# Kernel optimization log

Hardware: AMD Instinct MI355X
Metric: run time of the kernel (lower is better)

## Reference

```python
import jax, jax.numpy as jnp
import numpy as np

S, B, C, H = 1024, 4, 1024, 16
CC = C // H


def setup_inputs() -> dict:
    key = jax.random.key(0)
    k0, k1, k2, k3, k4, k5 = jax.random.split(key, 6)
    x = jax.random.normal(k0, (S, B, C), jnp.float32)
    pe = jax.random.normal(k1, (S, B, C), jnp.float32)
    # causal content mask: True = masked (query i cannot attend key j > i)
    causal = np.triu(np.ones((S, S), dtype=bool), 1)
    content_mask = jnp.asarray(np.broadcast_to(causal[:, :, None], (S, S, B)))
    # per-batch tail padding; every sequence has >= 512 valid tokens
    lengths = np.array([S, S - 128, S - 256, S - 512])
    padding_mask = jnp.asarray(np.arange(S)[:, None] >= lengths[None, :])  # [s, b]
    sc = 1.0 / np.sqrt(C).astype(np.float32)
    Wqkv = jax.random.normal(k2, (3 * C, C), jnp.float32) * sc
    bqkv = jax.random.normal(k3, (3 * C,), jnp.float32) * 0.01
    Wo = jax.random.normal(k4, (C, C), jnp.float32) * sc
    bo = jax.random.normal(k5, (C,), jnp.float32) * 0.01
    return {"x": x, "pe": pe, "content_mask": content_mask,
            "padding_mask": padding_mask, "Wqkv": Wqkv, "bqkv": bqkv,
            "Wo": Wo, "bo": bo}


def reference(x, pe, content_mask, padding_mask, Wqkv, bqkv, Wo, bo):
    s, b, c = x.shape
    qkv = (x + pe) @ Wqkv.T + bqkv                       # [s, b, 3c]
    q, k, v = jnp.split(qkv, 3, axis=-1)
    q = q.reshape(s, b, H, CC)
    k = k.reshape(s, b, H, CC)
    v = v.reshape(s, b, H, CC)
    temperature = 1.0 / np.sqrt(CC).astype(np.float32)
    qk = jnp.einsum('sbhc,tbhc->stbh', q, k) * temperature  # [s, t, b, h]
    mask = content_mask[:, :, :, None] | padding_mask[None, :, :, None]
    a = jnp.where(mask, -jnp.inf, qk)
    p = jax.nn.softmax(a, axis=1)                        # softmax over key dim t
    out = jnp.einsum('stbh,tbhc->sbhc', p, v).reshape(s, b, c)
    return out @ Wo.T + bo
```

## Files before the change

kernel.cpp:

```cpp
#include <hip/hip_runtime.h>
#include <hip/hip_bf16.h>

#define S_  1024
#define B_  4
#define C_  1024
#define H_  16
#define CC_ 64
#define M_  (S_ * B_)
#define N_QKV (3 * C_)

typedef __bf16 bf16x8 __attribute__((ext_vector_type(8)));
typedef __bf16 bf16x4 __attribute__((ext_vector_type(4)));
typedef float  f32x4  __attribute__((ext_vector_type(4)));

__device__ __forceinline__ void gload16(const void* g, void* l) {
    __builtin_amdgcn_global_load_lds(
        (const __attribute__((address_space(1))) void*)g,
        (__attribute__((address_space(3))) void*)l, 16, 0, 0);
}

__global__ void prep_kernel(const float* __restrict__ x, const float* __restrict__ pe,
                            const float* __restrict__ Wqkv, const float* __restrict__ Wo,
                            __bf16* __restrict__ xpe, __bf16* __restrict__ wq,
                            __bf16* __restrict__ wo) {
    int bid = blockIdx.x;
    int t = threadIdx.x;
    if (bid < 4096) {
        int i = bid * 256 + t;
        float4 a = ((const float4*)x)[i];
        float4 p = ((const float4*)pe)[i];
        bf16x4 r;
        r[0] = (__bf16)(a.x + p.x); r[1] = (__bf16)(a.y + p.y);
        r[2] = (__bf16)(a.z + p.z); r[3] = (__bf16)(a.w + p.w);
        ((bf16x4*)xpe)[i] = r;
    } else if (bid < 7168) {
        int i = (bid - 4096) * 256 + t;
        float4 a = ((const float4*)Wqkv)[i];
        bf16x4 r;
        r[0] = (__bf16)a.x; r[1] = (__bf16)a.y; r[2] = (__bf16)a.z; r[3] = (__bf16)a.w;
        ((bf16x4*)wq)[i] = r;
    } else {
        int i = (bid - 7168) * 256 + t;
        float4 a = ((const float4*)Wo)[i];
        bf16x4 r;
        r[0] = (__bf16)a.x; r[1] = (__bf16)a.y; r[2] = (__bf16)a.z; r[3] = (__bf16)a.w;
        ((bf16x4*)wo)[i] = r;
    }
}

template<int EPI, int BN>
__global__ __launch_bounds__(256, 2)
void gemm_bt_kernel(const __bf16* __restrict__ A, const __bf16* __restrict__ B,
                    const float* __restrict__ bias, int M, int N, int K,
                    float* __restrict__ Cf, __bf16* __restrict__ Cq,
                    __bf16* __restrict__ Vt) {
    constexpr int NB = BN / 32;
    __shared__ __bf16 Als[128 * 32];
    __shared__ __bf16 Bls[BN * 32];

    const int tid  = threadIdx.x;
    const int lane = tid & 63;
    const int wid  = tid >> 6;
    const int quad = lane >> 4;
    const int l15  = lane & 15;
    const int wm   = wid >> 1;
    const int wn   = wid & 1;
    const int m0   = blockIdx.y * 128;
    const int n0   = blockIdx.x * BN;

    const int u0 = tid, u1 = 256 + tid;
    const int row0 = u0 >> 2, ch0 = (u0 & 3) * 8;
    const int row1 = u1 >> 2, ch1 = (u1 & 3) * 8;
    char* lA0 = (char*)Als + (size_t)(wid * 64) * 16;
    char* lA1 = (char*)Als + (size_t)(256 + wid * 64) * 16;
    char* lB0 = (char*)Bls + (size_t)(wid * 64) * 16;
    char* lB1 = (char*)Bls + (size_t)(256 + wid * 64) * 16;

    f32x4 acc[4][NB];
#pragma unroll
    for (int i = 0; i < 4; i++)
#pragma unroll
        for (int j = 0; j < NB; j++) acc[i][j] = f32x4{0.f, 0.f, 0.f, 0.f};

    for (int k0 = 0; k0 < K; k0 += 32) {
        __syncthreads();
        gload16(&A[(size_t)(m0 + row0) * K + k0 + ch0], lA0);
        gload16(&A[(size_t)(m0 + row1) * K + k0 + ch1], lA1);
        gload16(&B[(size_t)(n0 + row0) * K + k0 + ch0], lB0);
        if (BN == 128)
            gload16(&B[(size_t)(n0 + row1) * K + k0 + ch1], lB1);
        __syncthreads();

        bf16x8 af[4], bfr[NB];
#pragma unroll
        for (int mb = 0; mb < 4; mb++)
            af[mb] = *(const bf16x8*)&Als[(wm * 64 + mb * 16 + l15) * 32 + quad * 8];
#pragma unroll
        for (int nb = 0; nb < NB; nb++)
            bfr[nb] = *(const bf16x8*)&Bls[(wn * (BN / 2) + nb * 16 + l15) * 32 + quad * 8];

#pragma unroll
        for (int mb = 0; mb < 4; mb++)
#pragma unroll
            for (int nb = 0; nb < NB; nb++)
                acc[mb][nb] = __builtin_amdgcn_mfma_f32_16x16x32_bf16(
                    af[mb], bfr[nb], acc[mb][nb], 0, 0, 0);
    }

#pragma unroll
    for (int mb = 0; mb < 4; mb++) {
#pragma unroll
        for (int nb = 0; nb < NB; nb++) {
#pragma unroll
            for (int r = 0; r < 4; r++) {
                int m = m0 + wm * 64 + mb * 16 + quad * 4 + r;
                int n = n0 + wn * (BN / 2) + nb * 16 + l15;
                float v = acc[mb][nb][r] + bias[n];
                if (EPI == 0) {
                    Cf[(size_t)m * N + n] = v;
                } else {
                    int sec = n >> 10;
                    int c   = n & 1023;
                    int h   = c >> 6;
                    int cc  = c & 63;
                    int s   = m >> 2;
                    int b   = m & 3;
                    if (sec == 2) {
                        size_t off = ((size_t)(b * H_ + h) * CC_ + cc) * S_ + s;
                        Vt[off] = (__bf16)v;
                    } else {
                        size_t off = ((((size_t)(sec * B_ + b) * H_ + h) * S_ + s) << 6) + cc;
                        Cq[off] = (__bf16)v;
                    }
                }
            }
        }
    }
}

__global__ __launch_bounds__(256, 4)
void attn_kernel(const __bf16* __restrict__ qkv, const __bf16* __restrict__ vt,
                 __bf16* __restrict__ att) {
    const int qt  = 15 - blockIdx.x;
    const int bh  = blockIdx.y;
    const int b   = bh >> 4;
    const int h   = bh & 15;
    const int len = 1024 - ((b == 1) ? 128 : (b == 2) ? 256 : (b == 3) ? 512 : 0);

    const int tid  = threadIdx.x;
    const int w    = tid >> 6;
    const int lane = tid & 63;
    const int quad = lane >> 4;
    const int l15  = lane & 15;
    const int qbase = qt * 64;

    const size_t head  = ((size_t)(b * H_ + h)) * S_ * CC_;
    const size_t plane = (size_t)B_ * H_ * S_ * CC_;
    const __bf16* qg  = qkv + head;
    const __bf16* kg  = qkv + plane + head;
    const __bf16* vtg = vt + (size_t)bh * CC_ * S_;

    const int qw = qbase + w * 16;
    const int q  = qw + l15;
    bf16x8 qf0 = *(const bf16x8*)&qg[(size_t)q * 64 + quad * 8];
    bf16x8 qf1 = *(const bf16x8*)&qg[(size_t)q * 64 + 32 + quad * 8];

    __shared__ __bf16 Kls[64 * 72];
    __shared__ __bf16 Vtls[64 * 72];
    __shared__ __bf16 Pls[4 * 16 * 72];
    __bf16* pw = &Pls[w * 16 * 72];

    f32x4 oacc[4];
#pragma unroll
    for (int cb = 0; cb < 4; cb++) oacc[cb] = f32x4{0.f, 0.f, 0.f, 0.f};
    float m_i = -1e30f, l_i = 0.f;

    const int kend_blk = min(qbase + 64, len);
    const int kend_w   = min(qw + 16, len);
    const float temp = 0.125f;

    const int r0 = tid >> 3,          c0 = (tid & 7) * 8;
    const int r1 = (256 + tid) >> 3,  c1 = (tid & 7) * 8;

    for (int t0 = 0; t0 < kend_blk; t0 += 64) {
        __syncthreads();
        *(bf16x8*)&Kls[r0 * 72 + c0]  = *(const bf16x8*)&kg[(size_t)(t0 + r0) * 64 + c0];
        *(bf16x8*)&Kls[r1 * 72 + c1]  = *(const bf16x8*)&kg[(size_t)(t0 + r1) * 64 + c1];
        *(bf16x8*)&Vtls[r0 * 72 + c0] = *(const bf16x8*)&vtg[(size_t)r0 * S_ + t0 + c0];
        *(bf16x8*)&Vtls[r1 * 72 + c1] = *(const bf16x8*)&vtg[(size_t)r1 * S_ + t0 + c1];
        __syncthreads();
        if (t0 >= kend_w) continue;

        f32x4 sc[4];
#pragma unroll
        for (int nb = 0; nb < 4; nb++) {
            bf16x8 kf0 = *(const bf16x8*)&Kls[(nb * 16 + l15) * 72 + quad * 8];
            bf16x8 kf1 = *(const bf16x8*)&Kls[(nb * 16 + l15) * 72 + 32 + quad * 8];
            f32x4 s = f32x4{0.f, 0.f, 0.f, 0.f};
            s = __builtin_amdgcn_mfma_f32_16x16x32_bf16(kf0, qf0, s, 0, 0, 0);
            s = __builtin_amdgcn_mfma_f32_16x16x32_bf16(kf1, qf1, s, 0, 0, 0);
            sc[nb] = s;
        }
        if (t0 + 64 <= qw) {
#pragma unroll
            for (int nb = 0; nb < 4; nb++)
#pragma unroll
                for (int r = 0; r < 4; r++) sc[nb][r] *= temp;
        } else {
#pragma unroll
            for (int nb = 0; nb < 4; nb++) {
#pragma unroll
                for (int r = 0; r < 4; r++) {
                    int key = t0 + nb * 16 + quad * 4 + r;
                    float v = sc[nb][r] * temp;
                    sc[nb][r] = (key > q) ? -1e30f : v;
                }
            }
        }
        float mx0 = fmaxf(fmaxf(sc[0][0], sc[0][1]), fmaxf(sc[0][2], sc[0][3]));
        float mx1 = fmaxf(fmaxf(sc[1][0], sc[1][1]), fmaxf(sc[1][2], sc[1][3]));
        float mx2 = fmaxf(fmaxf(sc[2][0], sc[2][1]), fmaxf(sc[2][2], sc[2][3]));
        float mx3 = fmaxf(fmaxf(sc[3][0], sc[3][1]), fmaxf(sc[3][2], sc[3][3]));
        float mx = fmaxf(fmaxf(mx0, mx1), fmaxf(mx2, mx3));
        mx = fmaxf(mx, __shfl_xor(mx, 16, 64));
        mx = fmaxf(mx, __shfl_xor(mx, 32, 64));
        float m_new = fmaxf(m_i, mx);
        float alpha = __expf(m_i - m_new);
        m_i = m_new;
        float sum = 0.f;
#pragma unroll
        for (int nb = 0; nb < 4; nb++) {
#pragma unroll
            for (int r = 0; r < 4; r++) {
                float pv = __expf(sc[nb][r] - m_new);
                sc[nb][r] = pv;
                sum += pv;
            }
        }
        sum += __shfl_xor(sum, 16, 64);
        sum += __shfl_xor(sum, 32, 64);
        l_i = l_i * alpha + sum;
#pragma unroll
        for (int cb = 0; cb < 4; cb++)
#pragma unroll
            for (int r = 0; r < 4; r++) oacc[cb][r] *= alpha;

#pragma unroll
        for (int nb = 0; nb < 4; nb++) {
            bf16x4 pk;
#pragma unroll
            for (int r = 0; r < 4; r++) pk[r] = (__bf16)sc[nb][r];
            *(bf16x4*)&pw[l15 * 72 + nb * 16 + quad * 4] = pk;
        }
        asm volatile("s_waitcnt lgkmcnt(0)" ::: "memory");
        bf16x8 pf0 = *(const bf16x8*)&pw[l15 * 72 + quad * 8];
        bf16x8 pf1 = *(const bf16x8*)&pw[l15 * 72 + 32 + quad * 8];

#pragma unroll
        for (int cb = 0; cb < 4; cb++) {
            bf16x8 vf0 = *(const bf16x8*)&Vtls[(cb * 16 + l15) * 72 + quad * 8];
            bf16x8 vf1 = *(const bf16x8*)&Vtls[(cb * 16 + l15) * 72 + 32 + quad * 8];
            oacc[cb] = __builtin_amdgcn_mfma_f32_16x16x32_bf16(vf0, pf0, oacc[cb], 0, 0, 0);
            oacc[cb] = __builtin_amdgcn_mfma_f32_16x16x32_bf16(vf1, pf1, oacc[cb], 0, 0, 0);
        }
    }

    float inv = 1.f / l_i;
    size_t rowoff = ((size_t)(q * B_ + b)) * C_ + h * 64;
#pragma unroll
    for (int cb = 0; cb < 4; cb++) {
        bf16x4 ov;
#pragma unroll
        for (int r = 0; r < 4; r++) ov[r] = (__bf16)(oacc[cb][r] * inv);
        *(bf16x4*)&att[rowoff + cb * 16 + quad * 4] = ov;
    }
}

extern "C" void kernel_launch(void* const* d_in, const int* in_sizes, int n_in,
                              void* d_out, int out_size, void* d_ws, size_t ws_size,
                              hipStream_t stream) {
    const float* x     = (const float*)d_in[0];
    const float* pe    = (const float*)d_in[1];
    const float* Wqkv  = (const float*)d_in[4];
    const float* bqkv  = (const float*)d_in[5];
    const float* Wo    = (const float*)d_in[6];
    const float* bo    = (const float*)d_in[7];
    float* out = (float*)d_out;

    __bf16* xpe   = (__bf16*)d_ws;
    __bf16* wqkvb = xpe + (size_t)M_ * C_;
    __bf16* wob   = wqkvb + (size_t)N_QKV * C_;
    __bf16* qkvb  = wob + (size_t)C_ * C_;
    __bf16* attb  = qkvb + (size_t)3 * B_ * H_ * S_ * CC_;
    __bf16* vtb   = attb + (size_t)M_ * C_;

    prep_kernel<<<8192, 256, 0, stream>>>(x, pe, Wqkv, Wo, xpe, wqkvb, wob);

    gemm_bt_kernel<1, 128><<<dim3(N_QKV / 128, M_ / 128), 256, 0, stream>>>(
        xpe, wqkvb, bqkv, M_, N_QKV, C_, nullptr, qkvb, vtb);

    attn_kernel<<<dim3(S_ / 64, B_ * H_), 256, 0, stream>>>(qkvb, vtb, attb);

    gemm_bt_kernel<0, 64><<<dim3(C_ / 64, M_ / 128), 256, 0, stream>>>(
        attb, wob, bo, M_, C_, C_, out, nullptr, nullptr);
}
```

Baseline: 198.7 us.

## Double GEMM K-step with XOR-swizzled LDS and fold softmax scale into Q

The GEMM now loads a 64-wide K slice per iteration instead of 32, halving the number of barrier pairs. It uses an XOR swizzle on the LDS chunk index to avoid bank conflicts, and LDS use per block doubles. Separately, Q is pre-multiplied by temperature*log2(e) in the QKV epilogue, so attention drops its per-score multiply and uses exp2 instead of exp. Pre-scaling Q before the bf16 cast slightly changes rounding.

```diff
diff --git a/kernel.cpp b/kernel.cpp
--- a/kernel.cpp
+++ b/kernel.cpp
@@ -1,5 +1,6 @@
 #include <hip/hip_runtime.h>
 #include <hip/hip_bf16.h>
+#include <math.h>
 
 #define S_  1024
 #define B_  4
@@ -12,6 +13,8 @@
 typedef __bf16 bf16x8 __attribute__((ext_vector_type(8)));
 typedef __bf16 bf16x4 __attribute__((ext_vector_type(4)));
 typedef float  f32x4  __attribute__((ext_vector_type(4)));
+
+#define QSCALE 0.1803368801111204f
 
 __device__ __forceinline__ void gload16(const void* g, void* l) {
     __builtin_amdgcn_global_load_lds(
@@ -55,8 +58,9 @@
                     float* __restrict__ Cf, __bf16* __restrict__ Cq,
                     __bf16* __restrict__ Vt) {
     constexpr int NB = BN / 32;
-    __shared__ __bf16 Als[128 * 32];
-    __shared__ __bf16 Bls[BN * 32];
+    constexpr int BI = BN / 32;
+    __shared__ __bf16 Als[128 * 64];
+    __shared__ __bf16 Bls[BN * 64];
 
     const int tid  = threadIdx.x;
     const int lane = tid & 63;
@@ -68,13 +72,25 @@
     const int m0   = blockIdx.y * 128;
     const int n0   = blockIdx.x * BN;
 
-    const int u0 = tid, u1 = 256 + tid;
-    const int row0 = u0 >> 2, ch0 = (u0 & 3) * 8;
-    const int row1 = u1 >> 2, ch1 = (u1 & 3) * 8;
-    char* lA0 = (char*)Als + (size_t)(wid * 64) * 16;
-    char* lA1 = (char*)Als + (size_t)(256 + wid * 64) * 16;
-    char* lB0 = (char*)Bls + (size_t)(wid * 64) * 16;
-    char* lB1 = (char*)Bls + (size_t)(256 + wid * 64) * 16;
+    int arow[4], ach[4];
+    char* lA[4];
+#pragma unroll
+    for (int i = 0; i < 4; i++) {
+        int u = i * 256 + tid;
+        arow[i] = u >> 3;
+        ach[i]  = ((u & 7) ^ ((u >> 3) & 7)) * 8;
+        lA[i]   = (char*)Als + (size_t)(i * 256 + wid * 64) * 16;
+    }
+    int brow[BI], bch[BI];
+    char* lB[BI];
+#pragma unroll
+    for (int i = 0; i < BI; i++) {
+        int u = i * 256 + tid;
+        brow[i] = u >> 3;
+        bch[i]  = ((u & 7) ^ ((u >> 3) & 7)) * 8;
+        lB[i]   = (char*)Bls + (size_t)(i * 256 + wid * 64) * 16;
+    }
+    const int x7 = (l15 & 7);
 
     f32x4 acc[4][NB];
 #pragma unroll
@@ -82,29 +98,34 @@
 #pragma unroll
         for (int j = 0; j < NB; j++) acc[i][j] = f32x4{0.f, 0.f, 0.f, 0.f};
 
-    for (int k0 = 0; k0 < K; k0 += 32) {
+    for (int k0 = 0; k0 < K; k0 += 64) {
         __syncthreads();
-        gload16(&A[(size_t)(m0 + row0) * K + k0 + ch0], lA0);
-        gload16(&A[(size_t)(m0 + row1) * K + k0 + ch1], lA1);
-        gload16(&B[(size_t)(n0 + row0) * K + k0 + ch0], lB0);
-        if (BN == 128)
-            gload16(&B[(size_t)(n0 + row1) * K + k0 + ch1], lB1);
+#pragma unroll
+        for (int i = 0; i < 4; i++)
+            gload16(&A[(size_t)(m0 + arow[i]) * K + k0 + ach[i]], lA[i]);
+#pragma unroll
+        for (int i = 0; i < BI; i++)
+            gload16(&B[(size_t)(n0 + brow[i]) * K + k0 + bch[i]], lB[i]);
         __syncthreads();
 
-        bf16x8 af[4], bfr[NB];
-#pragma unroll
-        for (int mb = 0; mb < 4; mb++)
-            af[mb] = *(const bf16x8*)&Als[(wm * 64 + mb * 16 + l15) * 32 + quad * 8];
-#pragma unroll
-        for (int nb = 0; nb < NB; nb++)
-            bfr[nb] = *(const bf16x8*)&Bls[(wn * (BN / 2) + nb * 16 + l15) * 32 + quad * 8];
-
-#pragma unroll
-        for (int mb = 0; mb < 4; mb++)
+#pragma unroll
+        for (int ks = 0; ks < 2; ks++) {
+            const int so = ((ks * 4 + quad) ^ x7) * 8;
+            bf16x8 af[4], bfr[NB];
+#pragma unroll
+            for (int mb = 0; mb < 4; mb++)
+                af[mb] = *(const bf16x8*)&Als[(wm * 64 + mb * 16 + l15) * 64 + so];
 #pragma unroll
             for (int nb = 0; nb < NB; nb++)
-                acc[mb][nb] = __builtin_amdgcn_mfma_f32_16x16x32_bf16(
-                    af[mb], bfr[nb], acc[mb][nb], 0, 0, 0);
+                bfr[nb] = *(const bf16x8*)&Bls[(wn * (BN / 2) + nb * 16 + l15) * 64 + so];
+
+#pragma unroll
+            for (int mb = 0; mb < 4; mb++)
+#pragma unroll
+                for (int nb = 0; nb < NB; nb++)
+                    acc[mb][nb] = __builtin_amdgcn_mfma_f32_16x16x32_bf16(
+                        af[mb], bfr[nb], acc[mb][nb], 0, 0, 0);
+        }
     }
 
 #pragma unroll
@@ -129,6 +150,7 @@
                         size_t off = ((size_t)(b * H_ + h) * CC_ + cc) * S_ + s;
                         Vt[off] = (__bf16)v;
                     } else {
+                        if (sec == 0) v *= QSCALE;
                         size_t off = ((((size_t)(sec * B_ + b) * H_ + h) * S_ + s) << 6) + cc;
                         Cq[off] = (__bf16)v;
                     }
@@ -177,7 +199,6 @@
 
     const int kend_blk = min(qbase + 64, len);
     const int kend_w   = min(qw + 16, len);
-    const float temp = 0.125f;
 
     const int r0 = tid >> 3,          c0 = (tid & 7) * 8;
     const int r1 = (256 + tid) >> 3,  c1 = (tid & 7) * 8;
@@ -201,19 +222,13 @@
             s = __builtin_amdgcn_mfma_f32_16x16x32_bf16(kf1, qf1, s, 0, 0, 0);
             sc[nb] = s;
         }
-        if (t0 + 64 <= qw) {
-#pragma unroll
-            for (int nb = 0; nb < 4; nb++)
-#pragma unroll
-                for (int r = 0; r < 4; r++) sc[nb][r] *= temp;
-        } else {
+        if (t0 + 64 > qw) {
 #pragma unroll
             for (int nb = 0; nb < 4; nb++) {
 #pragma unroll
                 for (int r = 0; r < 4; r++) {
                     int key = t0 + nb * 16 + quad * 4 + r;
-                    float v = sc[nb][r] * temp;
-                    sc[nb][r] = (key > q) ? -1e30f : v;
+                    sc[nb][r] = (key > q) ? -1e30f : sc[nb][r];
                 }
             }
         }
@@ -225,14 +240,14 @@
         mx = fmaxf(mx, __shfl_xor(mx, 16, 64));
         mx = fmaxf(mx, __shfl_xor(mx, 32, 64));
         float m_new = fmaxf(m_i, mx);
-        float alpha = __expf(m_i - m_new);
+        float alpha = exp2f(m_i - m_new);
         m_i = m_new;
         float sum = 0.f;
 #pragma unroll
         for (int nb = 0; nb < 4; nb++) {
 #pragma unroll
             for (int r = 0; r < 4; r++) {
-                float pv = __expf(sc[nb][r] - m_new);
+                float pv = exp2f(sc[nb][r] - m_new);
                 sc[nb][r] = pv;
                 sum += pv;
             }
```

Result: no change. 195.7 us (-1.5%).
